# Kernel optimization log

Hardware: AMD Instinct MI355X
Metric: run time of the kernel (lower is better)

The kernel has to match this reference:

```python
import jax, jax.numpy as jnp
import numpy as np

B, T, C, K = 256, 336, 512, 3
CLAMP_LO, CLAMP_HI = 1e-4, 1.0 - 1e-4


def setup_inputs() -> dict:
    key = jax.random.key(0)
    k1, k2 = jax.random.split(key)
    x = jax.random.normal(k1, (B, T, C), dtype=jnp.float32)
    # learned params: logit_alpha [K, C], mix_logits [C, K]
    # initialize logit_alpha near logit(init_alphas) with small noise so sigmoid(.) stays ~[0.75, 0.99]
    init_alphas = jnp.array([0.8, 0.9, 0.98], dtype=jnp.float32)
    base = jnp.log(init_alphas / (1.0 - init_alphas))  # logit
    logit_alpha = base[:, None] + 0.05 * jax.random.normal(k2, (K, C), dtype=jnp.float32)
    mix_logits = jnp.zeros((C, K), dtype=jnp.float32)
    return {"x": x, "logit_alpha": logit_alpha, "mix_logits": mix_logits}


def reference(x, logit_alpha, mix_logits):
    Bx, Tx, Cx = x.shape
    a = jnp.clip(jax.nn.sigmoid(logit_alpha), CLAMP_LO, CLAMP_HI).astype(x.dtype)  # [K, C]
    t_idx = jnp.arange(Tx, dtype=x.dtype)[:, None, None]                          # [T, 1, 1]
    a_pow = a[None, :, :] ** t_idx                                                # [T, K, C]
    # weights: a^t, multiplied by (1 - a) for t >= 1
    scale = jnp.where(t_idx > 0, 1.0 - a[None, :, :], jnp.ones_like(a)[None])     # [T, K, C]
    weights = a_pow * scale                                                       # [T, K, C]
    divisor = jnp.maximum(a_pow, 1e-8)                                            # [T, K, C]
    xw = x[:, :, None, :] * weights[None]                                         # [B, T, K, C]
    yk = jnp.cumsum(xw, axis=1) / divisor[None]                                   # [B, T, K, C]
    mix = jax.nn.softmax(mix_logits.astype(x.dtype), axis=-1).T                   # [K, C]
    trend = jnp.sum(yk * mix[None, None, :, :], axis=2)                           # [B, T, C]
    return trend
```

## Files before the change

### kernel.cpp

```cpp
#include <hip/hip_runtime.h>

namespace {
constexpr int kB = 256;
constexpr int kT = 336;
constexpr int kC = 512;
constexpr int kK = 3;
constexpr int kUnroll = 8;
}

__global__ __launch_bounds__(256) void ema_mix_kernel(
    const float* __restrict__ x,
    const float* __restrict__ logit_alpha,
    const float* __restrict__ mix_logits,
    float* __restrict__ out)
{
    const int c = ((blockIdx.x & 1) << 8) | threadIdx.x;
    const int b = blockIdx.x >> 1;

    float a[kK], oma[kK], inva[kK], mixw[kK];
    {
        float logits[kK];
        float lmax = -3.402823e38f;
        #pragma unroll
        for (int k = 0; k < kK; ++k) {
            logits[k] = mix_logits[c * kK + k];
            lmax = fmaxf(lmax, logits[k]);
        }
        float esum = 0.f;
        #pragma unroll
        for (int k = 0; k < kK; ++k) {
            logits[k] = expf(logits[k] - lmax);
            esum += logits[k];
        }
        const float rs = 1.0f / esum;
        #pragma unroll
        for (int k = 0; k < kK; ++k) {
            mixw[k] = logits[k] * rs;
            const float z = logit_alpha[k * kC + c];
            float s;
            if (z >= 0.f) {
                s = 1.0f / (1.0f + expf(-z));
            } else {
                const float e = expf(z);
                s = e / (1.0f + e);
            }
            s = fminf(fmaxf(s, 1e-4f), (float)(1.0 - 1e-4));
            a[k]    = s;
            oma[k]  = 1.0f - s;
            inva[k] = 1.0f / s;
        }
    }

    const float* xp = x   + (size_t)b * (kT * kC) + c;
    float*       op = out + (size_t)b * (kT * kC) + c;

    float apow[kK], vinv[kK], S[kK];
    #pragma unroll
    for (int k = 0; k < kK; ++k) { apow[k] = 1.f; vinv[k] = 1.f; S[k] = 0.f; }

    float xcur[kUnroll];
    #pragma unroll
    for (int i = 0; i < kUnroll; ++i) xcur[i] = xp[i * kC];

    for (int tc = 0; tc < kT; tc += kUnroll) {
        const bool more = (tc + kUnroll < kT);
        float xnxt[kUnroll];
        if (more) {
            #pragma unroll
            for (int i = 0; i < kUnroll; ++i) xnxt[i] = xp[(tc + kUnroll + i) * kC];
        }
        #pragma unroll
        for (int i = 0; i < kUnroll; ++i) {
            const int t = tc + i;
            const float xv = xcur[i];
            float o = 0.f;
            #pragma unroll
            for (int k = 0; k < kK; ++k) {
                const float w = (t == 0) ? 1.0f : apow[k] * oma[k];
                S[k] = fmaf(xv, w, S[k]);
                const float inv = fminf(vinv[k], 1e8f);
                o = fmaf(S[k] * mixw[k], inv, o);
                apow[k] *= a[k];
                vinv[k] *= inva[k];
            }
            op[t * kC] = o;
        }
        if (more) {
            #pragma unroll
            for (int i = 0; i < kUnroll; ++i) xcur[i] = xnxt[i];
        }
    }
}

extern "C" void kernel_launch(void* const* d_in, const int* in_sizes, int n_in,
                              void* d_out, int out_size, void* d_ws, size_t ws_size,
                              hipStream_t stream) {
    const float* x  = (const float*)d_in[0];
    const float* la = (const float*)d_in[1];
    const float* ml = (const float*)d_in[2];
    float* o = (float*)d_out;

    const int blocks = kB * (kC / 256);
    ema_mix_kernel<<<dim3(blocks), dim3(256), 0, stream>>>(x, la, ml, o);
}
```

Before: 72.07 us.

## Split time axis into chunks with two-pass scan and shared-memory carry

Each block now handles 64 channels with four threads per channel, each owning a quarter of the time axis. A first pass computes per-chunk weighted sums, exchanged through shared memory as prefix carries, and a second pass recomputes the running scan and writes outputs. This raises parallelism from 131k to 524k threads to hide the serial dependency and memory latency, at the cost of reading x twice, adding a barrier, and starting powers with powf, which may differ slightly numerically.

```diff
diff --git a/kernel.cpp b/kernel.cpp
--- a/kernel.cpp
+++ b/kernel.cpp
@@ -1,11 +1,13 @@
 #include <hip/hip_runtime.h>
 
 namespace {
-constexpr int kB = 256;
-constexpr int kT = 336;
-constexpr int kC = 512;
-constexpr int kK = 3;
-constexpr int kUnroll = 8;
+constexpr int kB      = 256;
+constexpr int kT      = 336;
+constexpr int kC      = 512;
+constexpr int kK      = 3;
+constexpr int kChunks = 4;
+constexpr int kTc     = kT / kChunks;
+constexpr int kCTile  = 64;
 }
 
 __global__ __launch_bounds__(256) void ema_mix_kernel(
@@ -14,8 +16,14 @@
     const float* __restrict__ mix_logits,
     float* __restrict__ out)
 {
-    const int c = ((blockIdx.x & 1) << 8) | threadIdx.x;
-    const int b = blockIdx.x >> 1;
+    __shared__ float s_tot[kK][kChunks][kCTile];
+
+    const int tid = threadIdx.x;
+    const int ci  = tid & (kCTile - 1);
+    const int j   = tid >> 6;
+    const int c0  = (blockIdx.x & 7) << 6;
+    const int b   = blockIdx.x >> 3;
+    const int c   = c0 + ci;
 
     float a[kK], oma[kK], inva[kK], mixw[kK];
     {
@@ -51,43 +59,65 @@
         }
     }
 
-    const float* xp = x   + (size_t)b * (kT * kC) + c;
-    float*       op = out + (size_t)b * (kT * kC) + c;
+    const int t0 = j * kTc;
+    float ap0[kK], vi0[kK];
+    #pragma unroll
+    for (int k = 0; k < kK; ++k) {
+        ap0[k] = powf(a[k], (float)t0);
+        vi0[k] = 1.0f / ap0[k];
+    }
 
-    float apow[kK], vinv[kK], S[kK];
+    const float* xp = x   + ((size_t)b * kT + t0) * kC + c;
+    float*       op = out + ((size_t)b * kT + t0) * kC + c;
+
+    float Tk[kK] = {0.f, 0.f, 0.f};
+    {
+        float ap[kK];
+        #pragma unroll
+        for (int k = 0; k < kK; ++k) ap[k] = ap0[k];
+        #pragma unroll 4
+        for (int i = 0; i < kTc; ++i) {
+            const float xv = xp[(size_t)i * kC];
+            const int t = t0 + i;
+            #pragma unroll
+            for (int k = 0; k < kK; ++k) {
+                const float w = (t == 0) ? 1.0f : ap[k] * oma[k];
+                Tk[k] = fmaf(xv, w, Tk[k]);
+                ap[k] *= a[k];
+            }
+        }
+    }
     #pragma unroll
-    for (int k = 0; k < kK; ++k) { apow[k] = 1.f; vinv[k] = 1.f; S[k] = 0.f; }
+    for (int k = 0; k < kK; ++k) s_tot[k][j][ci] = Tk[k];
+    __syncthreads();
 
-    float xcur[kUnroll];
+    float O[kK] = {0.f, 0.f, 0.f};
     #pragma unroll
-    for (int i = 0; i < kUnroll; ++i) xcur[i] = xp[i * kC];
+    for (int k = 0; k < kK; ++k) {
+        #pragma unroll
+        for (int jj = 0; jj < kChunks - 1; ++jj) {
+            if (jj < j) O[k] += s_tot[k][jj][ci];
+        }
+    }
 
-    for (int tc = 0; tc < kT; tc += kUnroll) {
-        const bool more = (tc + kUnroll < kT);
-        float xnxt[kUnroll];
-        if (more) {
-            #pragma unroll
-            for (int i = 0; i < kUnroll; ++i) xnxt[i] = xp[(tc + kUnroll + i) * kC];
-        }
+    {
+        float ap[kK], vi[kK], S[kK];
         #pragma unroll
-        for (int i = 0; i < kUnroll; ++i) {
-            const int t = tc + i;
-            const float xv = xcur[i];
+        for (int k = 0; k < kK; ++k) { ap[k] = ap0[k]; vi[k] = vi0[k]; S[k] = O[k]; }
+        #pragma unroll 4
+        for (int i = 0; i < kTc; ++i) {
+            const float xv = xp[(size_t)i * kC];
+            const int t = t0 + i;
             float o = 0.f;
             #pragma unroll
             for (int k = 0; k < kK; ++k) {
-                const float w = (t == 0) ? 1.0f : apow[k] * oma[k];
+                const float w = (t == 0) ? 1.0f : ap[k] * oma[k];
                 S[k] = fmaf(xv, w, S[k]);
-                const float inv = fminf(vinv[k], 1e8f);
-                o = fmaf(S[k] * mixw[k], inv, o);
-                apow[k] *= a[k];
-                vinv[k] *= inva[k];
+                o = fmaf(S[k] * mixw[k], fminf(vi[k], 1e8f), o);
+                ap[k] *= a[k];
+                vi[k] *= inva[k];
             }
-            op[t * kC] = o;
-        }
-        if (more) {
-            #pragma unroll
-            for (int i = 0; i < kUnroll; ++i) xcur[i] = xnxt[i];
+            op[(size_t)i * kC] = o;
         }
     }
 }
@@ -100,6 +130,6 @@
     const float* ml = (const float*)d_in[2];
     float* o = (float*)d_out;
 
-    const int blocks = kB * (kC / 256);
+    const int blocks = kB * (kC / kCTile);
     ema_mix_kernel<<<dim3(blocks), dim3(256), 0, stream>>>(x, la, ml, o);
 }
```

Measured after the change: 93.60 us. 29.9% more time.
